# Kernel tuning notes

Hardware: AMD Instinct MI355X
Metric: run time of the kernel (lower is better)

Reference implementation:

```python
import jax, jax.numpy as jnp
import numpy as np

B, N, C = 2, 8192, 768
H, K = 12, 256
D = C // H
HID = 4 * C
EPS = 1e-6

def layer_norm(x, w, b):
    mu = jnp.mean(x, axis=-1, keepdims=True)
    var = jnp.mean(jnp.square(x - mu), axis=-1, keepdims=True)
    return (x - mu) * jax.lax.rsqrt(var + EPS) * w + b

def setup_inputs() -> dict:
    key = jax.random.key(0)
    ks = jax.random.split(key, 8)
    s = 0.02
    return {
        "x": jax.random.normal(ks[0], (B, N, C), jnp.float32),
        "ln1_w": jnp.ones((C,), jnp.float32),
        "ln1_b": jnp.zeros((C,), jnp.float32),
        "qkv_w": jax.random.normal(ks[1], (C, 3 * C), jnp.float32) * s,
        "qkv_b": jnp.zeros((3 * C,), jnp.float32),
        "Ek": jax.random.normal(ks[2], (N, K), jnp.float32) * s,
        "Ev": jax.random.normal(ks[3], (N, K), jnp.float32) * s,
        "proj_w": jax.random.normal(ks[4], (C, C), jnp.float32) * s,
        "proj_b": jnp.zeros((C,), jnp.float32),
        "ln2_w": jnp.ones((C,), jnp.float32),
        "ln2_b": jnp.zeros((C,), jnp.float32),
        "fc1_w": jax.random.normal(ks[5], (C, HID), jnp.float32) * s,
        "fc1_b": jnp.zeros((HID,), jnp.float32),
        "fc2_w": jax.random.normal(ks[6], (HID, C), jnp.float32) * s,
        "fc2_b": jnp.zeros((C,), jnp.float32),
    }

def reference(x, ln1_w, ln1_b, qkv_w, qkv_b, Ek, Ev, proj_w, proj_b,
              ln2_w, ln2_b, fc1_w, fc1_b, fc2_w, fc2_b):
    scale = D ** -0.5
    # --- attention branch ---
    h = layer_norm(x, ln1_w, ln1_b)
    qkv = h @ qkv_w + qkv_b                      # (B,N,3C)
    qkv = qkv.reshape(B, N, 3, H, D).transpose(2, 0, 3, 1, 4)  # (3,B,H,N,D)
    q, k, v = qkv[0], qkv[1], qkv[2]
    # Linformer: project K/V along sequence dim N -> K
    k_proj = jnp.einsum('bhnd,nk->bhkd', k, Ek)
    v_proj = jnp.einsum('bhnd,nk->bhkd', v, Ev)
    logits = jnp.einsum('bhnd,bhkd->bhnk', q, k_proj) * scale
    logits = jnp.clip(logits, -50.0, 50.0)
    attn = jax.nn.softmax(logits, axis=-1)
    o = jnp.einsum('bhnk,bhkd->bhnd', attn, v_proj)
    o = o.transpose(0, 2, 1, 3).reshape(B, N, C)
    o = o @ proj_w + proj_b
    x = x + o                                    # alpha_attn = 1.0
    # --- MLP branch ---
    h = layer_norm(x, ln2_w, ln2_b)
    h = jax.nn.gelu(h @ fc1_w + fc1_b, approximate=False)
    h = h @ fc2_w + fc2_b
    return x + h                                 # alpha_mlp = 1.0
```

## Files before the change

kernel.cpp:

```cpp
#include <hip/hip_runtime.h>
#include <cstdint>

#define DEV __device__ __forceinline__

typedef __bf16 bf16x8 __attribute__((ext_vector_type(8)));
typedef float f32x4 __attribute__((ext_vector_type(4)));

DEV uint16_t f2bf(float f) {
  uint32_t u = __float_as_uint(f);
  u += 0x7FFFu + ((u >> 16) & 1u);
  return (uint16_t)(u >> 16);
}
DEV float bf2f(uint16_t h) { return __uint_as_float(((uint32_t)h) << 16); }

DEV void gload16(const void* g, void* l) {
  __builtin_amdgcn_global_load_lds((const __attribute__((address_space(1))) void*)g,
                                   (__attribute__((address_space(3))) void*)l, 16, 0, 0);
}

template <int N> DEV void waitcnt_vm() {
  if constexpr (N == 0) asm volatile("s_waitcnt vmcnt(0)" ::: "memory");
  else if constexpr (N == 4) asm volatile("s_waitcnt vmcnt(4)" ::: "memory");
  else if constexpr (N == 6) asm volatile("s_waitcnt vmcnt(6)" ::: "memory");
  else static_assert(N == 0 || N == 4 || N == 6, "unsupported vmcnt");
}

DEV float gelu_f(float v) {
  float u = v * (0.7978845608f + 0.0356774081f * v * v);
  return v / (1.f + __expf(-2.f * u));
}

__global__ __launch_bounds__(256) void ln768(const float* __restrict__ x,
                                             const float* __restrict__ w,
                                             const float* __restrict__ b,
                                             uint16_t* __restrict__ out) {
  const size_t row = blockIdx.x;
  const float* xr = x + row * 768;
  const int t = threadIdx.x;
  float v0 = xr[t], v1 = xr[t + 256], v2 = xr[t + 512];
  float s = v0 + v1 + v2;
  float s2 = v0 * v0 + v1 * v1 + v2 * v2;
#pragma unroll
  for (int o = 32; o; o >>= 1) {
    s += __shfl_down(s, o);
    s2 += __shfl_down(s2, o);
  }
  __shared__ float sh[8];
  if ((t & 63) == 0) { sh[t >> 6] = s; sh[4 + (t >> 6)] = s2; }
  __syncthreads();
  s = sh[0] + sh[1] + sh[2] + sh[3];
  s2 = sh[4] + sh[5] + sh[6] + sh[7];
  const float mu = s * (1.f / 768.f);
  const float var = s2 * (1.f / 768.f) - mu * mu;
  const float rstd = rsqrtf(var + 1e-6f);
  uint16_t* orow = out + row * 768;
  orow[t]       = f2bf((v0 - mu) * rstd * w[t] + b[t]);
  orow[t + 256] = f2bf((v1 - mu) * rstd * w[t + 256] + b[t + 256]);
  orow[t + 512] = f2bf((v2 - mu) * rstd * w[t + 512] + b[t + 512]);
}

__global__ __launch_bounds__(256) void transpose_f2b(const float* __restrict__ in,
                                                     uint16_t* __restrict__ outp,
                                                     int ldin, int ldout) {
  __shared__ float tile[32][33];
  const int tx = threadIdx.x, ty = threadIdx.y;
  const size_t x = (size_t)blockIdx.x * 32 + tx;
  const size_t y = (size_t)blockIdx.y * 32 + ty;
#pragma unroll
  for (int j = 0; j < 4; ++j) tile[ty + j * 8][tx] = in[(y + j * 8) * ldin + x];
  __syncthreads();
  const size_t x2 = (size_t)blockIdx.y * 32 + tx;
  const size_t y2 = (size_t)blockIdx.x * 32 + ty;
#pragma unroll
  for (int j = 0; j < 4; ++j) outp[(y2 + j * 8) * ldout + x2] = f2bf(tile[tx][ty + j * 8]);
}

__global__ __launch_bounds__(256) void transpose_b2b(const uint16_t* __restrict__ in,
                                                     uint16_t* __restrict__ outp,
                                                     int ldin, int ldout) {
  __shared__ uint16_t tile[32][33];
  const int tx = threadIdx.x, ty = threadIdx.y;
  const size_t x = (size_t)blockIdx.x * 32 + tx;
  const size_t y = (size_t)blockIdx.y * 32 + ty;
#pragma unroll
  for (int j = 0; j < 4; ++j) tile[ty + j * 8][tx] = in[(y + j * 8) * ldin + x];
  __syncthreads();
  const size_t x2 = (size_t)blockIdx.y * 32 + tx;
  const size_t y2 = (size_t)blockIdx.x * 32 + ty;
#pragma unroll
  for (int j = 0; j < 4; ++j) outp[(y2 + j * 8) * ldout + x2] = tile[tx][ty + j * 8];
}

__global__ __launch_bounds__(256) void rowsum512(const uint16_t* __restrict__ ekv,
                                                 float* __restrict__ colsum) {
  const int row = blockIdx.x * 4 + (threadIdx.x >> 6);
  const int lane = threadIdx.x & 63;
  const uint16_t* r = ekv + (size_t)row * 8192 + lane * 8;
  float s = 0.f;
#pragma unroll
  for (int it = 0; it < 16; ++it) {
    bf16x8 v = *(const bf16x8*)(r + it * 512);
#pragma unroll
    for (int j = 0; j < 8; ++j) s += (float)v[j];
  }
#pragma unroll
  for (int o = 32; o; o >>= 1) s += __shfl_down(s, o);
  if (lane == 0) colsum[row] = s;
}

__global__ __launch_bounds__(256) void kv_reduce(const float* __restrict__ part,
                                                 uint16_t* __restrict__ hkv) {
  const int i = blockIdx.x * 256 + threadIdx.x;
  float s = part[i] + part[786432 + i] + part[2 * 786432 + i] + part[3 * 786432 + i];
  hkv[i] = f2bf(s);
}

template <int BM, int BN, bool OUTBF, bool HASBIAS, bool DOGELU, bool HASRES, bool HASRS>
__global__ __launch_bounds__(256) void gemm_nt(
    const uint16_t* __restrict__ Abase, const uint16_t* __restrict__ Bbase,
    void* __restrict__ Cbase, const float* __restrict__ bias,
    const float* __restrict__ resbase, const float* __restrict__ rowscale,
    int Kd, int lda, int ldb, int ldc,
    int zdiv, size_t sAhi, size_t sAlo, size_t sBhi, size_t sBlo,
    size_t sChi, size_t sClo, int rs_z, int bias_z) {
  const int z = blockIdx.z;
  const int zhi = z / zdiv, zlo = z - zhi * zdiv;
  const uint16_t* A = Abase + zhi * sAhi + zlo * sAlo;
  const uint16_t* B = Bbase + zhi * sBhi + zlo * sBlo;
  const size_t coff = zhi * sChi + zlo * sClo;

  constexpr int WTM = BM / 2, WTN = BN / 2;
  constexpr int FM = WTM / 16, FN = WTN / 16;
  const int tid = threadIdx.x;
  const int wave = tid >> 6, lane = tid & 63;
  const int wm = wave >> 1, wn = wave & 1;
  const int l16 = lane & 15, lhi = lane >> 4;

  __shared__ __align__(16) uint16_t sA[BM * 32];
  __shared__ __align__(16) uint16_t sB[BN * 32];

  f32x4 acc[FM][FN];
#pragma unroll
  for (int m = 0; m < FM; ++m)
#pragma unroll
    for (int n = 0; n < FN; ++n) acc[m][n] = f32x4{0.f, 0.f, 0.f, 0.f};

  const int row0 = blockIdx.x * BM;
  const int col0 = blockIdx.y * BN;
  const int rr = tid >> 2, cq = tid & 3;

  for (int k0 = 0; k0 < Kd; k0 += 32) {
    __syncthreads();
#pragma unroll
    for (int is = 0; is < BM / 64; ++is) {
      const uint16_t* g = A + (size_t)(row0 + is * 64 + rr) * lda + k0 + cq * 8;
      gload16(g, &sA[is * 2048 + tid * 8]);
    }
#pragma unroll
    for (int is = 0; is < BN / 64; ++is) {
      const uint16_t* g = B + (size_t)(col0 + is * 64 + rr) * ldb + k0 + cq * 8;
      gload16(g, &sB[is * 2048 + tid * 8]);
    }
    __syncthreads();

    bf16x8 af[FM], bq[FN];
#pragma unroll
    for (int m = 0; m < FM; ++m)
      af[m] = *(const bf16x8*)(&sA[(wm * WTM + m * 16 + l16) * 32 + lhi * 8]);
#pragma unroll
    for (int n = 0; n < FN; ++n)
      bq[n] = *(const bf16x8*)(&sB[(wn * WTN + n * 16 + l16) * 32 + lhi * 8]);
#pragma unroll
    for (int m = 0; m < FM; ++m)
#pragma unroll
      for (int n = 0; n < FN; ++n)
        acc[m][n] = __builtin_amdgcn_mfma_f32_16x16x32_bf16(af[m], bq[n], acc[m][n], 0, 0, 0);
  }

  float* Cf = (float*)Cbase;
  uint16_t* Cb = (uint16_t*)Cbase;
#pragma unroll
  for (int m = 0; m < FM; ++m) {
#pragma unroll
    for (int n = 0; n < FN; ++n) {
      const int col = col0 + wn * WTN + n * 16 + l16;
      float bv = 0.f;
      if (HASBIAS) bv = bias[zlo * bias_z + col];
#pragma unroll
      for (int r = 0; r < 4; ++r) {
        const int row = row0 + wm * WTM + m * 16 + lhi * 4 + r;
        float v = acc[m][n][r];
        if (HASBIAS) {
          if (HASRS) v += rowscale[zlo * rs_z + row] * bv;
          else v += bv;
        }
        if (DOGELU) v = gelu_f(v);
        const size_t cidx = coff + (size_t)row * ldc + col;
        if (HASRES) v += resbase[cidx];
        if (OUTBF) Cb[cidx] = f2bf(v);
        else Cf[cidx] = v;
      }
    }
  }
}

__global__ __launch_bounds__(256, 3) void attn_fused(
    const uint16_t* __restrict__ q,
    const uint16_t* __restrict__ kproj,
    const uint16_t* __restrict__ vprojT,
    uint16_t* __restrict__ o) {
  const int bh = blockIdx.y;
  const int b = bh / 12, h = bh % 12;
  const int n0 = blockIdx.x * 64;
  const int tid = threadIdx.x, wave = tid >> 6, lane = tid & 63;
  const int l16 = lane & 15, lhi = lane >> 4;
  const int wm = wave >> 1, wn = wave & 1;

  __shared__ __align__(16) uint16_t sP[64 * 256];
  __shared__ float redm[2][64], reds[2][64], recs[64];

  const uint16_t* Kp = kproj + (size_t)b * 196608 + h * 64;
  const uint16_t* Qp = q + ((size_t)b * 8192 + n0) * 768 + h * 64;
  const uint16_t* Vp = vprojT + ((size_t)b * 768 + h * 64) * 256;

  f32x4 st[8][2];
#pragma unroll
  for (int m = 0; m < 8; ++m)
#pragma unroll
    for (int nf = 0; nf < 2; ++nf) st[m][nf] = f32x4{0.f, 0.f, 0.f, 0.f};
#pragma unroll
  for (int ks = 0; ks < 2; ++ks) {
    bf16x8 kf[8], qf[2];
#pragma unroll
    for (int m = 0; m < 8; ++m) {
      const int kvi = wm * 128 + m * 16 + l16;
      kf[m] = *(const bf16x8*)(Kp + (size_t)kvi * 768 + ks * 32 + lhi * 8);
    }
#pragma unroll
    for (int nf = 0; nf < 2; ++nf) {
      const int n = wn * 32 + nf * 16 + l16;
      qf[nf] = *(const bf16x8*)(Qp + (size_t)n * 768 + ks * 32 + lhi * 8);
    }
#pragma unroll
    for (int m = 0; m < 8; ++m)
#pragma unroll
      for (int nf = 0; nf < 2; ++nf)
        st[m][nf] = __builtin_amdgcn_mfma_f32_16x16x32_bf16(kf[m], qf[nf], st[m][nf], 0, 0, 0);
  }

  float pmax[2] = {-50.f, -50.f};
#pragma unroll
  for (int m = 0; m < 8; ++m)
#pragma unroll
    for (int nf = 0; nf < 2; ++nf)
#pragma unroll
      for (int r = 0; r < 4; ++r) {
        float v = fminf(fmaxf(st[m][nf][r] * 0.125f, -50.f), 50.f);
        st[m][nf][r] = v;
        pmax[nf] = fmaxf(pmax[nf], v);
      }
#pragma unroll
  for (int nf = 0; nf < 2; ++nf) {
    pmax[nf] = fmaxf(pmax[nf], __shfl_xor(pmax[nf], 16));
    pmax[nf] = fmaxf(pmax[nf], __shfl_xor(pmax[nf], 32));
  }
  if (lhi == 0) {
#pragma unroll
    for (int nf = 0; nf < 2; ++nf) redm[wm][wn * 32 + nf * 16 + l16] = pmax[nf];
  }
  __syncthreads();
  float M[2];
#pragma unroll
  for (int nf = 0; nf < 2; ++nf) {
    const int col = wn * 32 + nf * 16 + l16;
    M[nf] = fmaxf(redm[0][col], redm[1][col]);
  }

  float psum[2] = {0.f, 0.f};
#pragma unroll
  for (int m = 0; m < 8; ++m) {
#pragma unroll
    for (int nf = 0; nf < 2; ++nf) {
      float e0 = __expf(st[m][nf][0] - M[nf]);
      float e1 = __expf(st[m][nf][1] - M[nf]);
      float e2 = __expf(st[m][nf][2] - M[nf]);
      float e3 = __expf(st[m][nf][3] - M[nf]);
      psum[nf] += (e0 + e1) + (e2 + e3);
      uint2 pk;
      pk.x = (uint32_t)f2bf(e0) | ((uint32_t)f2bf(e1) << 16);
      pk.y = (uint32_t)f2bf(e2) | ((uint32_t)f2bf(e3) << 16);
      const int n = wn * 32 + nf * 16 + l16;
      const int kvb2 = (wm * 128 + m * 16 + lhi * 4) * 2;
      *(uint2*)((char*)sP + n * 512 + (kvb2 ^ ((n & 7) << 4))) = pk;
    }
  }
#pragma unroll
  for (int nf = 0; nf < 2; ++nf) {
    psum[nf] += __shfl_xor(psum[nf], 16);
    psum[nf] += __shfl_xor(psum[nf], 32);
  }
  if (lhi == 0) {
#pragma unroll
    for (int nf = 0; nf < 2; ++nf) reds[wm][wn * 32 + nf * 16 + l16] = psum[nf];
  }
  __syncthreads();
  if (wm == 0 && lhi == 0) {
#pragma unroll
    for (int nf = 0; nf < 2; ++nf) {
      const int col = wn * 32 + nf * 16 + l16;
      recs[col] = 1.f / (reds[0][col] + reds[1][col]);
    }
  }
  __syncthreads();

  f32x4 pacc[2][2];
#pragma unroll
  for (int mf = 0; mf < 2; ++mf)
#pragma unroll
    for (int nf = 0; nf < 2; ++nf) pacc[mf][nf] = f32x4{0.f, 0.f, 0.f, 0.f};
#pragma unroll
  for (int ks = 0; ks < 8; ++ks) {
    bf16x8 pa[2], vb[2];
#pragma unroll
    for (int mf = 0; mf < 2; ++mf) {
      const int n = wm * 32 + mf * 16 + l16;
      pa[mf] = *(const bf16x8*)((char*)sP + n * 512 + ((ks * 64 + lhi * 16) ^ ((n & 7) << 4)));
    }
#pragma unroll
    for (int nf = 0; nf < 2; ++nf) {
      const int d = wn * 32 + nf * 16 + l16;
      vb[nf] = *(const bf16x8*)(Vp + (size_t)d * 256 + ks * 32 + lhi * 8);
    }
#pragma unroll
    for (int mf = 0; mf < 2; ++mf)
#pragma unroll
      for (int nf = 0; nf < 2; ++nf)
        pacc[mf][nf] = __builtin_amdgcn_mfma_f32_16x16x32_bf16(pa[mf], vb[nf], pacc[mf][nf], 0, 0, 0);
  }
  uint16_t* orow = o + ((size_t)b * 8192 + n0) * 768 + h * 64;
#pragma unroll
  for (int mf = 0; mf < 2; ++mf) {
#pragma unroll
    for (int r = 0; r < 4; ++r) {
      const int n = wm * 32 + mf * 16 + lhi * 4 + r;
      const float inv = recs[n];
#pragma unroll
      for (int nf = 0; nf < 2; ++nf) {
        const int d = wn * 32 + nf * 16 + l16;
        orow[(size_t)n * 768 + d] = f2bf(pacc[mf][nf][r] * inv);
      }
    }
  }
}

template <bool OUTBF, bool HASBIAS, bool DOGELU, bool HASRES>
__global__ __launch_bounds__(256, 3) void gemm128(
    const uint16_t* __restrict__ A, const uint16_t* __restrict__ B,
    void* __restrict__ Cbase, const float* __restrict__ bias,
    const float* __restrict__ res, int Kd, int lda, int ldb, int ldc) {
  constexpr int PL = 4096;
  __shared__ __align__(16) uint16_t lds[3 * 2 * PL];

  const int nn = gridDim.y;
  const int nwg = gridDim.x * gridDim.y;
  const int bid = blockIdx.y * gridDim.x + blockIdx.x;
  const int q = nwg >> 3, r8 = nwg & 7, xcd = bid & 7, idx = bid >> 3;
  const int wg = (xcd < r8 ? xcd * (q + 1) : r8 * (q + 1) + (xcd - r8) * q) + idx;
  const int bm = wg / nn, bn = wg % nn;
  const int row0 = bm * 128, col0 = bn * 128;

  const int tid = threadIdx.x;
  const int wave = tid >> 6, lane = tid & 63;
  const int wm = wave >> 1, wn = wave & 1;
  const int l16 = lane & 15, lhi = lane >> 4;
  const int srow = tid >> 2, sq = tid & 3;

  auto stage = [&](int buf, int t) {
    const int k0 = t * 32;
    uint16_t* sa = lds + buf * 2 * PL;
#pragma unroll
    for (int j = 0; j < 2; ++j) {
      const int rw = j * 64 + srow;
      const int sl = sq ^ ((rw >> 1) & 3);
      gload16(A + (size_t)(row0 + rw) * lda + k0 + sl * 8, sa + rw * 32 + sq * 8);
    }
#pragma unroll
    for (int j = 0; j < 2; ++j) {
      const int rw = j * 64 + srow;
      const int sl = sq ^ ((rw >> 1) & 3);
      gload16(B + (size_t)(col0 + rw) * ldb + k0 + sl * 8, sa + PL + rw * 32 + sq * 8);
    }
  };

  f32x4 acc[4][4];
#pragma unroll
  for (int m = 0; m < 4; ++m)
#pragma unroll
    for (int n = 0; n < 4; ++n) acc[m][n] = f32x4{0.f, 0.f, 0.f, 0.f};

  const int NT = Kd >> 5;
  stage(0, 0);
  stage(1, 1);

  for (int t = 0; t < NT; ++t) {
    if (t < NT - 1) waitcnt_vm<4>();
    else waitcnt_vm<0>();
    __builtin_amdgcn_s_barrier();
    asm volatile("" ::: "memory");
    if (t + 2 < NT) stage((t + 2) % 3, t + 2);

    const uint16_t* sa = lds + (t % 3) * 2 * PL;
    const uint16_t* sb = sa + PL;
    bf16x8 af[4], bfv[4];
#pragma unroll
    for (int n = 0; n < 4; ++n) {
      const int rw = wn * 64 + n * 16 + l16;
      bfv[n] = *(const bf16x8*)(sb + rw * 32 + (lhi ^ ((rw >> 1) & 3)) * 8);
    }
#pragma unroll
    for (int m = 0; m < 4; ++m) {
      const int rw = wm * 64 + m * 16 + l16;
      af[m] = *(const bf16x8*)(sa + rw * 32 + (lhi ^ ((rw >> 1) & 3)) * 8);
    }
    __builtin_amdgcn_s_setprio(1);
#pragma unroll
    for (int m = 0; m < 4; ++m)
#pragma unroll
      for (int n = 0; n < 4; ++n)
        acc[m][n] = __builtin_amdgcn_mfma_f32_16x16x32_bf16(af[m], bfv[n], acc[m][n], 0, 0, 0);
    __builtin_amdgcn_s_setprio(0);
  }

  float* Cf = (float*)Cbase;
  uint16_t* Cb = (uint16_t*)Cbase;
#pragma unroll
  for (int m = 0; m < 4; ++m) {
#pragma unroll
    for (int n = 0; n < 4; ++n) {
      const int col = col0 + wn * 64 + n * 16 + l16;
      float bv = 0.f;
      if (HASBIAS) bv = bias[col];
#pragma unroll
      for (int r = 0; r < 4; ++r) {
        const int row = row0 + wm * 64 + m * 16 + lhi * 4 + r;
        float v = acc[m][n][r] + bv;
        if (DOGELU) v = gelu_f(v);
        const size_t cidx = (size_t)row * ldc + col;
        if (HASRES) v += res[cidx];
        if (OUTBF) Cb[cidx] = f2bf(v);
        else Cf[cidx] = v;
      }
    }
  }
}

template <bool OUTBF, bool HASBIAS, bool DOGELU, bool HASRES>
__global__ __launch_bounds__(256, 2) void gemm256n(
    const uint16_t* __restrict__ A, const uint16_t* __restrict__ B,
    void* __restrict__ Cbase, const float* __restrict__ bias,
    const float* __restrict__ res, int Kd, int lda, int ldb, int ldc) {
  constexpr int APL = 8192, BPL = 4096;
  __shared__ __align__(16) uint16_t lds[3 * (APL + BPL)];

  const int nn = gridDim.y;
  const int nwg = gridDim.x * gridDim.y;
  const int bid = blockIdx.y * gridDim.x + blockIdx.x;
  const int q = nwg >> 3, r8 = nwg & 7, xcd = bid & 7, idx = bid >> 3;
  const int wg = (xcd < r8 ? xcd * (q + 1) : r8 * (q + 1) + (xcd - r8) * q) + idx;
  const int bm = wg / nn, bn = wg % nn;
  const int row0 = bm * 256, col0 = bn * 128;

  const int tid = threadIdx.x;
  const int wave = tid >> 6, lane = tid & 63;
  const int wm = wave >> 1, wn = wave & 1;
  const int l16 = lane & 15, lhi = lane >> 4;
  const int srow = tid >> 2, sq = tid & 3;

  auto stage = [&](int buf, int t) {
    const int k0 = t * 32;
    uint16_t* sa = lds + buf * (APL + BPL);
#pragma unroll
    for (int j = 0; j < 4; ++j) {
      const int rw = j * 64 + srow;
      const int sl = sq ^ ((rw >> 1) & 3);
      gload16(A + (size_t)(row0 + rw) * lda + k0 + sl * 8, sa + rw * 32 + sq * 8);
    }
#pragma unroll
    for (int j = 0; j < 2; ++j) {
      const int rw = j * 64 + srow;
      const int sl = sq ^ ((rw >> 1) & 3);
      gload16(B + (size_t)(col0 + rw) * ldb + k0 + sl * 8, sa + APL + rw * 32 + sq * 8);
    }
  };

  f32x4 acc[8][4];
#pragma unroll
  for (int m = 0; m < 8; ++m)
#pragma unroll
    for (int n = 0; n < 4; ++n) acc[m][n] = f32x4{0.f, 0.f, 0.f, 0.f};

  const int NT = Kd >> 5;
  stage(0, 0);
  stage(1, 1);

  for (int t = 0; t < NT; ++t) {
    if (t < NT - 1) waitcnt_vm<6>();
    else waitcnt_vm<0>();
    __builtin_amdgcn_s_barrier();
    asm volatile("" ::: "memory");
    if (t + 2 < NT) stage((t + 2) % 3, t + 2);

    const uint16_t* sa = lds + (t % 3) * (APL + BPL);
    const uint16_t* sb = sa + APL;
    bf16x8 af[8], bfv[4];
#pragma unroll
    for (int n = 0; n < 4; ++n) {
      const int rw = wn * 64 + n * 16 + l16;
      bfv[n] = *(const bf16x8*)(sb + rw * 32 + (lhi ^ ((rw >> 1) & 3)) * 8);
    }
#pragma unroll
    for (int m = 0; m < 8; ++m) {
      const int rw = wm * 128 + m * 16 + l16;
      af[m] = *(const bf16x8*)(sa + rw * 32 + (lhi ^ ((rw >> 1) & 3)) * 8);
    }
    __builtin_amdgcn_s_setprio(1);
#pragma unroll
    for (int m = 0; m < 8; ++m)
#pragma unroll
      for (int n = 0; n < 4; ++n)
        acc[m][n] = __builtin_amdgcn_mfma_f32_16x16x32_bf16(af[m], bfv[n], acc[m][n], 0, 0, 0);
    __builtin_amdgcn_s_setprio(0);
  }

  float* Cf = (float*)Cbase;
  uint16_t* Cb = (uint16_t*)Cbase;
#pragma unroll
  for (int m = 0; m < 8; ++m) {
#pragma unroll
    for (int n = 0; n < 4; ++n) {
      const int col = col0 + wn * 64 + n * 16 + l16;
      float bv = 0.f;
      if (HASBIAS) bv = bias[col];
#pragma unroll
      for (int r = 0; r < 4; ++r) {
        const int row = row0 + wm * 128 + m * 16 + lhi * 4 + r;
        float v = acc[m][n][r] + bv;
        if (DOGELU) v = gelu_f(v);
        const size_t cidx = (size_t)row * ldc + col;
        if (HASRES) v += res[cidx];
        if (OUTBF) Cb[cidx] = f2bf(v);
        else Cf[cidx] = v;
      }
    }
  }
}

extern "C" void kernel_launch(void* const* d_in, const int* in_sizes, int n_in,
                              void* d_out, int out_size, void* d_ws, size_t ws_size,
                              hipStream_t stream) {
  const float* x      = (const float*)d_in[0];
  const float* ln1_w  = (const float*)d_in[1];
  const float* ln1_b  = (const float*)d_in[2];
  const float* qkv_w  = (const float*)d_in[3];
  const float* qkv_b  = (const float*)d_in[4];
  const float* Ek     = (const float*)d_in[5];
  const float* Ev     = (const float*)d_in[6];
  const float* proj_w = (const float*)d_in[7];
  const float* proj_b = (const float*)d_in[8];
  const float* ln2_w  = (const float*)d_in[9];
  const float* ln2_b  = (const float*)d_in[10];
  const float* fc1_w  = (const float*)d_in[11];
  const float* fc1_b  = (const float*)d_in[12];
  const float* fc2_w  = (const float*)d_in[13];
  const float* fc2_b  = (const float*)d_in[14];
  float* out = (float*)d_out;

  char* w8 = (char*)d_ws;
  size_t off = 0;
  auto take = [&](size_t bytes) { char* p = w8 + off; off += bytes; return p; };
  uint16_t* qkv_wT  = (uint16_t*)take(2304ull * 768 * 2);
  uint16_t* proj_wT = (uint16_t*)take(768ull * 768 * 2);
  uint16_t* fc1_wT  = (uint16_t*)take(3072ull * 768 * 2);
  uint16_t* fc2_wT  = (uint16_t*)take(768ull * 3072 * 2);
  uint16_t* EkT     = (uint16_t*)take(256ull * 8192 * 2);
  uint16_t* EvT     = (uint16_t*)take(256ull * 8192 * 2);
  uint16_t* h_bf    = (uint16_t*)take(16384ull * 768 * 2);
  uint16_t* hT      = (uint16_t*)take(2ull * 768 * 8192 * 2);
  uint16_t* q_bf    = (uint16_t*)take(16384ull * 768 * 2);
  uint16_t* big     = (uint16_t*)take(100663296ull);
  uint16_t* hkv_bf  = (uint16_t*)take(2ull * 512 * 768 * 2);
  uint16_t* kproj   = (uint16_t*)take(4ull * 256 * 768 * 2);
  uint16_t* vprojT  = (uint16_t*)take(2ull * 768 * 256 * 2);
  uint16_t* o_bf    = (uint16_t*)take(16384ull * 768 * 2);
  float* colsum     = (float*)take(512 * 4);
  float* part = (float*)big;
  (void)ws_size; (void)in_sizes; (void)n_in; (void)out_size;

  const dim3 tb(32, 8);
  transpose_f2b<<<dim3(72, 24), tb, 0, stream>>>(qkv_w, qkv_wT, 2304, 768);
  transpose_f2b<<<dim3(24, 24), tb, 0, stream>>>(proj_w, proj_wT, 768, 768);
  transpose_f2b<<<dim3(96, 24), tb, 0, stream>>>(fc1_w, fc1_wT, 3072, 768);
  transpose_f2b<<<dim3(24, 96), tb, 0, stream>>>(fc2_w, fc2_wT, 768, 3072);
  transpose_f2b<<<dim3(8, 256), tb, 0, stream>>>(Ek, EkT, 256, 8192);
  transpose_f2b<<<dim3(8, 256), tb, 0, stream>>>(Ev, EvT, 256, 8192);
  ln768<<<16384, 256, 0, stream>>>(x, ln1_w, ln1_b, h_bf);
  for (int b = 0; b < 2; ++b)
    transpose_b2b<<<dim3(24, 256), tb, 0, stream>>>(
        h_bf + (size_t)b * 8192 * 768, hT + (size_t)b * 768 * 8192, 768, 8192);
  rowsum512<<<128, 256, 0, stream>>>(EkT, colsum);
  gemm128<true, true, false, false><<<dim3(128, 6), 256, 0, stream>>>(
      h_bf, qkv_wT, q_bf, qkv_b, nullptr, 768, 768, 768, 768);
  gemm_nt<64, 64, false, false, false, false, false><<<dim3(8, 12, 8), 256, 0, stream>>>(
      EkT, hT, part, nullptr, nullptr, nullptr, 2048, 8192, 8192, 768,
      4, 0, 2048, 768ull * 8192, 2048, 393216, 786432, 0, 0);
  kv_reduce<<<3072, 256, 0, stream>>>(part, hkv_bf);
  gemm_nt<64, 64, true, true, false, false, true><<<dim3(4, 12, 4), 256, 0, stream>>>(
      hkv_bf, qkv_wT + 768ull * 768, kproj, qkv_b + 768, nullptr, colsum,
      768, 768, 768, 768,
      2, 512ull * 768, 256ull * 768, 0, 768ull * 768, 196608, 393216, 256, 768);
  for (int b = 0; b < 2; ++b)
    transpose_b2b<<<dim3(24, 8), tb, 0, stream>>>(
        kproj + (size_t)(2 + b) * 196608, vprojT + (size_t)b * 768 * 256, 768, 256);
  attn_fused<<<dim3(128, 24), 256, 0, stream>>>(q_bf, kproj, vprojT, o_bf);
  gemm128<false, true, false, true><<<dim3(128, 6), 256, 0, stream>>>(
      o_bf, proj_wT, out, proj_b, x, 768, 768, 768, 768);
  ln768<<<16384, 256, 0, stream>>>(out, ln2_w, ln2_b, h_bf);
  gemm256n<true, true, true, false><<<dim3(64, 24), 256, 0, stream>>>(
      h_bf, fc1_wT, big, fc1_b, nullptr, 768, 768, 768, 3072);
  gemm256n<false, true, false, true><<<dim3(64, 6), 256, 0, stream>>>(
      big, fc2_wT, out, fc2_b, out, 3072, 3072, 3072, 768);
}
```

Baseline: 473.3 us.

## Drop h and V-proj transposes, add direct hkv kernel, retune MLP GEMMs

Removes the transposes of the normalized activations and of the projected V. A new hkv_tn kernel reads E^T and row-major h directly, with strided scalar gathers into MFMA fragments. The K/V weight GEMM now writes V-proj already transposed. The fc1 GEMM moves to 512-thread blocks with smaller per-wave tiles, and fc2 moves to the gemm128 kernel. These cut extra passes over memory and kernel launches, but the new strided 2-byte loads in hkv_tn lack LDS staging and may be poorly coalesced.

```diff
diff --git a/kernel.cpp b/kernel.cpp
--- a/kernel.cpp
+++ b/kernel.cpp
@@ -20,9 +20,9 @@
 
 template <int N> DEV void waitcnt_vm() {
   if constexpr (N == 0) asm volatile("s_waitcnt vmcnt(0)" ::: "memory");
+  else if constexpr (N == 3) asm volatile("s_waitcnt vmcnt(3)" ::: "memory");
   else if constexpr (N == 4) asm volatile("s_waitcnt vmcnt(4)" ::: "memory");
-  else if constexpr (N == 6) asm volatile("s_waitcnt vmcnt(6)" ::: "memory");
-  else static_assert(N == 0 || N == 4 || N == 6, "unsupported vmcnt");
+  else static_assert(N == 0 || N == 3 || N == 4, "unsupported vmcnt");
 }
 
 DEV float gelu_f(float v) {
@@ -75,22 +75,6 @@
   for (int j = 0; j < 4; ++j) outp[(y2 + j * 8) * ldout + x2] = f2bf(tile[tx][ty + j * 8]);
 }
 
-__global__ __launch_bounds__(256) void transpose_b2b(const uint16_t* __restrict__ in,
-                                                     uint16_t* __restrict__ outp,
-                                                     int ldin, int ldout) {
-  __shared__ uint16_t tile[32][33];
-  const int tx = threadIdx.x, ty = threadIdx.y;
-  const size_t x = (size_t)blockIdx.x * 32 + tx;
-  const size_t y = (size_t)blockIdx.y * 32 + ty;
-#pragma unroll
-  for (int j = 0; j < 4; ++j) tile[ty + j * 8][tx] = in[(y + j * 8) * ldin + x];
-  __syncthreads();
-  const size_t x2 = (size_t)blockIdx.y * 32 + tx;
-  const size_t y2 = (size_t)blockIdx.x * 32 + ty;
-#pragma unroll
-  for (int j = 0; j < 4; ++j) outp[(y2 + j * 8) * ldout + x2] = tile[tx][ty + j * 8];
-}
-
 __global__ __launch_bounds__(256) void rowsum512(const uint16_t* __restrict__ ekv,
                                                  float* __restrict__ colsum) {
   const int row = blockIdx.x * 4 + (threadIdx.x >> 6);
@@ -108,6 +92,61 @@
   if (lane == 0) colsum[row] = s;
 }
 
+__global__ __launch_bounds__(256) void hkv_tn(const uint16_t* __restrict__ ET,
+                                              const uint16_t* __restrict__ h,
+                                              float* __restrict__ part) {
+  const int bid = blockIdx.x;
+  const int wg = (bid & 7) * 96 + (bid >> 3);
+  const int inner = wg & 31;
+  const int kt = inner & 7, ns = inner >> 3;
+  const int rest = wg >> 5;
+  const int ct = rest % 12, b = rest / 12;
+  const int k0 = kt * 64, c0 = ct * 64, nsb = ns * 2048;
+
+  const int tid = threadIdx.x, wave = tid >> 6, lane = tid & 63;
+  const int l16 = lane & 15, lhi = lane >> 4;
+  const int wm = wave >> 1, wn = wave & 1;
+
+  f32x4 acc[2][2];
+#pragma unroll
+  for (int m = 0; m < 2; ++m)
+#pragma unroll
+    for (int n = 0; n < 2; ++n) acc[m][n] = f32x4{0.f, 0.f, 0.f, 0.f};
+
+  const uint16_t* Eb = ET + (size_t)(k0 + wm * 32 + l16) * 8192 + nsb + lhi * 8;
+  const uint16_t* Hb = h + ((size_t)b * 8192 + nsb + lhi * 8) * 768 + c0 + wn * 32 + l16;
+
+  for (int n0 = 0; n0 < 2048; n0 += 32) {
+    bf16x8 ef[2];
+    ef[0] = *(const bf16x8*)(Eb + n0);
+    ef[1] = *(const bf16x8*)(Eb + 16 * 8192 + n0);
+    bf16x8 vf[2];
+#pragma unroll
+    for (int nf = 0; nf < 2; ++nf) {
+      const uint16_t* p = Hb + (size_t)n0 * 768 + nf * 16;
+      union { bf16x8 v; uint16_t u[8]; } tu;
+#pragma unroll
+      for (int j = 0; j < 8; ++j) tu.u[j] = p[(size_t)j * 768];
+      vf[nf] = tu.v;
+    }
+#pragma unroll
+    for (int m = 0; m < 2; ++m)
+#pragma unroll
+      for (int nf = 0; nf < 2; ++nf)
+        acc[m][nf] = __builtin_amdgcn_mfma_f32_16x16x32_bf16(ef[m], vf[nf], acc[m][nf], 0, 0, 0);
+  }
+
+  float* outp = part + ((size_t)ns * 2 + b) * 393216;
+#pragma unroll
+  for (int m = 0; m < 2; ++m)
+#pragma unroll
+    for (int nf = 0; nf < 2; ++nf)
+#pragma unroll
+      for (int r = 0; r < 4; ++r)
+        outp[(size_t)(k0 + wm * 32 + m * 16 + lhi * 4 + r) * 768 + c0 + wn * 32 + nf * 16 + l16] =
+            acc[m][nf][r];
+}
+
 __global__ __launch_bounds__(256) void kv_reduce(const float* __restrict__ part,
                                                  uint16_t* __restrict__ hkv) {
   const int i = blockIdx.x * 256 + threadIdx.x;
@@ -115,11 +154,11 @@
   hkv[i] = f2bf(s);
 }
 
-template <int BM, int BN, bool OUTBF, bool HASBIAS, bool DOGELU, bool HASRES, bool HASRS>
-__global__ __launch_bounds__(256) void gemm_nt(
+template <int BM, int BN>
+__global__ __launch_bounds__(256) void gemm_kvw(
     const uint16_t* __restrict__ Abase, const uint16_t* __restrict__ Bbase,
-    void* __restrict__ Cbase, const float* __restrict__ bias,
-    const float* __restrict__ resbase, const float* __restrict__ rowscale,
+    uint16_t* __restrict__ Cbase, const float* __restrict__ bias,
+    const float* __restrict__ rowscale, uint16_t* __restrict__ vpt,
     int Kd, int lda, int ldb, int ldc,
     int zdiv, size_t sAhi, size_t sAlo, size_t sBhi, size_t sBlo,
     size_t sChi, size_t sClo, int rs_z, int bias_z) {
@@ -177,28 +216,21 @@
         acc[m][n] = __builtin_amdgcn_mfma_f32_16x16x32_bf16(af[m], bq[n], acc[m][n], 0, 0, 0);
   }
 
-  float* Cf = (float*)Cbase;
-  uint16_t* Cb = (uint16_t*)Cbase;
 #pragma unroll
   for (int m = 0; m < FM; ++m) {
 #pragma unroll
     for (int n = 0; n < FN; ++n) {
       const int col = col0 + wn * WTN + n * 16 + l16;
-      float bv = 0.f;
-      if (HASBIAS) bv = bias[zlo * bias_z + col];
+      const float bv = bias[zlo * bias_z + col];
 #pragma unroll
       for (int r = 0; r < 4; ++r) {
         const int row = row0 + wm * WTM + m * 16 + lhi * 4 + r;
-        float v = acc[m][n][r];
-        if (HASBIAS) {
-          if (HASRS) v += rowscale[zlo * rs_z + row] * bv;
-          else v += bv;
+        float v = acc[m][n][r] + rowscale[zlo * rs_z + row] * bv;
+        if (zlo == 1) {
+          vpt[(size_t)zhi * 196608 + (size_t)col * 256 + row] = f2bf(v);
+        } else {
+          Cbase[coff + (size_t)row * ldc + col] = f2bf(v);
         }
-        if (DOGELU) v = gelu_f(v);
-        const size_t cidx = coff + (size_t)row * ldc + col;
-        if (HASRES) v += resbase[cidx];
-        if (OUTBF) Cb[cidx] = f2bf(v);
-        else Cf[cidx] = v;
       }
     }
   }
@@ -455,7 +487,7 @@
 }
 
 template <bool OUTBF, bool HASBIAS, bool DOGELU, bool HASRES>
-__global__ __launch_bounds__(256, 2) void gemm256n(
+__global__ __launch_bounds__(512, 4) void gemm512(
     const uint16_t* __restrict__ A, const uint16_t* __restrict__ B,
     void* __restrict__ Cbase, const float* __restrict__ bias,
     const float* __restrict__ res, int Kd, int lda, int ldb, int ldc) {
@@ -480,22 +512,21 @@
     const int k0 = t * 32;
     uint16_t* sa = lds + buf * (APL + BPL);
 #pragma unroll
-    for (int j = 0; j < 4; ++j) {
-      const int rw = j * 64 + srow;
+    for (int j = 0; j < 2; ++j) {
+      const int rw = j * 128 + srow;
       const int sl = sq ^ ((rw >> 1) & 3);
       gload16(A + (size_t)(row0 + rw) * lda + k0 + sl * 8, sa + rw * 32 + sq * 8);
     }
-#pragma unroll
-    for (int j = 0; j < 2; ++j) {
-      const int rw = j * 64 + srow;
+    {
+      const int rw = srow;
       const int sl = sq ^ ((rw >> 1) & 3);
       gload16(B + (size_t)(col0 + rw) * ldb + k0 + sl * 8, sa + APL + rw * 32 + sq * 8);
     }
   };
 
-  f32x4 acc[8][4];
-#pragma unroll
-  for (int m = 0; m < 8; ++m)
+  f32x4 acc[4][4];
+#pragma unroll
+  for (int m = 0; m < 4; ++m)
 #pragma unroll
     for (int n = 0; n < 4; ++n) acc[m][n] = f32x4{0.f, 0.f, 0.f, 0.f};
 
@@ -504,7 +535,7 @@
   stage(1, 1);
 
   for (int t = 0; t < NT; ++t) {
-    if (t < NT - 1) waitcnt_vm<6>();
+    if (t < NT - 1) waitcnt_vm<3>();
     else waitcnt_vm<0>();
     __builtin_amdgcn_s_barrier();
     asm volatile("" ::: "memory");
@@ -512,20 +543,20 @@
 
     const uint16_t* sa = lds + (t % 3) * (APL + BPL);
     const uint16_t* sb = sa + APL;
-    bf16x8 af[8], bfv[4];
+    bf16x8 af[4], bfv[4];
 #pragma unroll
     for (int n = 0; n < 4; ++n) {
       const int rw = wn * 64 + n * 16 + l16;
       bfv[n] = *(const bf16x8*)(sb + rw * 32 + (lhi ^ ((rw >> 1) & 3)) * 8);
     }
 #pragma unroll
-    for (int m = 0; m < 8; ++m) {
-      const int rw = wm * 128 + m * 16 + l16;
+    for (int m = 0; m < 4; ++m) {
+      const int rw = wm * 64 + m * 16 + l16;
       af[m] = *(const bf16x8*)(sa + rw * 32 + (lhi ^ ((rw >> 1) & 3)) * 8);
     }
     __builtin_amdgcn_s_setprio(1);
 #pragma unroll
-    for (int m = 0; m < 8; ++m)
+    for (int m = 0; m < 4; ++m)
 #pragma unroll
       for (int n = 0; n < 4; ++n)
         acc[m][n] = __builtin_amdgcn_mfma_f32_16x16x32_bf16(af[m], bfv[n], acc[m][n], 0, 0, 0);
@@ -535,7 +566,7 @@
   float* Cf = (float*)Cbase;
   uint16_t* Cb = (uint16_t*)Cbase;
 #pragma unroll
-  for (int m = 0; m < 8; ++m) {
+  for (int m = 0; m < 4; ++m) {
 #pragma unroll
     for (int n = 0; n < 4; ++n) {
       const int col = col0 + wn * 64 + n * 16 + l16;
@@ -543,7 +574,7 @@
       if (HASBIAS) bv = bias[col];
 #pragma unroll
       for (int r = 0; r < 4; ++r) {
-        const int row = row0 + wm * 128 + m * 16 + lhi * 4 + r;
+        const int row = row0 + wm * 64 + m * 16 + lhi * 4 + r;
         float v = acc[m][n][r] + bv;
         if (DOGELU) v = gelu_f(v);
         const size_t cidx = (size_t)row * ldc + col;
@@ -585,11 +616,10 @@
   uint16_t* EkT     = (uint16_t*)take(256ull * 8192 * 2);
   uint16_t* EvT     = (uint16_t*)take(256ull * 8192 * 2);
   uint16_t* h_bf    = (uint16_t*)take(16384ull * 768 * 2);
-  uint16_t* hT      = (uint16_t*)take(2ull * 768 * 8192 * 2);
   uint16_t* q_bf    = (uint16_t*)take(16384ull * 768 * 2);
   uint16_t* big     = (uint16_t*)take(100663296ull);
   uint16_t* hkv_bf  = (uint16_t*)take(2ull * 512 * 768 * 2);
-  uint16_t* kproj   = (uint16_t*)take(4ull * 256 * 768 * 2);
+  uint16_t* kproj   = (uint16_t*)take(2ull * 256 * 768 * 2);
   uint16_t* vprojT  = (uint16_t*)take(2ull * 768 * 256 * 2);
   uint16_t* o_bf    = (uint16_t*)take(16384ull * 768 * 2);
   float* colsum     = (float*)take(512 * 4);
@@ -603,30 +633,22 @@
   transpose_f2b<<<dim3(24, 96), tb, 0, stream>>>(fc2_w, fc2_wT, 768, 3072);
   transpose_f2b<<<dim3(8, 256), tb, 0, stream>>>(Ek, EkT, 256, 8192);
   transpose_f2b<<<dim3(8, 256), tb, 0, stream>>>(Ev, EvT, 256, 8192);
+  rowsum512<<<128, 256, 0, stream>>>(EkT, colsum);
   ln768<<<16384, 256, 0, stream>>>(x, ln1_w, ln1_b, h_bf);
-  for (int b = 0; b < 2; ++b)
-    transpose_b2b<<<dim3(24, 256), tb, 0, stream>>>(
-        h_bf + (size_t)b * 8192 * 768, hT + (size_t)b * 768 * 8192, 768, 8192);
-  rowsum512<<<128, 256, 0, stream>>>(EkT, colsum);
   gemm128<true, true, false, false><<<dim3(128, 6), 256, 0, stream>>>(
       h_bf, qkv_wT, q_bf, qkv_b, nullptr, 768, 768, 768, 768);
-  gemm_nt<64, 64, false, false, false, false, false><<<dim3(8, 12, 8), 256, 0, stream>>>(
-      EkT, hT, part, nullptr, nullptr, nullptr, 2048, 8192, 8192, 768,
-      4, 0, 2048, 768ull * 8192, 2048, 393216, 786432, 0, 0);
+  hkv_tn<<<768, 256, 0, stream>>>(EkT, h_bf, part);
   kv_reduce<<<3072, 256, 0, stream>>>(part, hkv_bf);
-  gemm_nt<64, 64, true, true, false, false, true><<<dim3(4, 12, 4), 256, 0, stream>>>(
-      hkv_bf, qkv_wT + 768ull * 768, kproj, qkv_b + 768, nullptr, colsum,
+  gemm_kvw<64, 64><<<dim3(4, 12, 4), 256, 0, stream>>>(
+      hkv_bf, qkv_wT + 768ull * 768, kproj, qkv_b + 768, colsum, vprojT,
       768, 768, 768, 768,
-      2, 512ull * 768, 256ull * 768, 0, 768ull * 768, 196608, 393216, 256, 768);
-  for (int b = 0; b < 2; ++b)
-    transpose_b2b<<<dim3(24, 8), tb, 0, stream>>>(
-        kproj + (size_t)(2 + b) * 196608, vprojT + (size_t)b * 768 * 256, 768, 256);
+      2, 512ull * 768, 256ull * 768, 0, 768ull * 768, 196608, 0, 256, 768);
   attn_fused<<<dim3(128, 24), 256, 0, stream>>>(q_bf, kproj, vprojT, o_bf);
   gemm128<false, true, false, true><<<dim3(128, 6), 256, 0, stream>>>(
       o_bf, proj_wT, out, proj_b, x, 768, 768, 768, 768);
   ln768<<<16384, 256, 0, stream>>>(out, ln2_w, ln2_b, h_bf);
-  gemm256n<true, true, true, false><<<dim3(64, 24), 256, 0, stream>>>(
+  gemm512<true, true, true, false><<<dim3(64, 24), 512, 0, stream>>>(
       h_bf, fc1_wT, big, fc1_b, nullptr, 768, 768, 768, 3072);
-  gemm256n<false, true, false, true><<<dim3(64, 6), 256, 0, stream>>>(
+  gemm128<false, true, false, true><<<dim3(128, 6), 256, 0, stream>>>(
       big, fc2_wT, out, fc2_b, out, 3072, 3072, 3072, 768);
 }
```

New measurement: 467.1 us. About the same (-1.3%).
